# Optimization experiments

Measured on AMD Instinct MI355X. Metric: run time of the kernel, lower is better.

## Reference

```python
import jax, jax.numpy as jnp
import numpy as np

B = 16
PATCH_NUM = 32      # L of inter branch
PATCH_SIZE = 128    # L of intra branch
WIN_SIZE = PATCH_NUM * PATCH_SIZE  # 4096
H = 8
E = 64


def setup_inputs() -> dict:
    key = jax.random.key(0)
    ks = jax.random.split(key, 6)
    return {
        "q_inter": jax.random.normal(ks[0], (B, PATCH_NUM, H, E), jnp.float32),
        "k_inter": jax.random.normal(ks[1], (B, PATCH_NUM, H, E), jnp.float32),
        "v_inter": jax.random.normal(ks[2], (B, PATCH_NUM, H, E), jnp.float32),
        "q_intra": jax.random.normal(ks[3], (B, PATCH_SIZE, H, E), jnp.float32),
        "k_intra": jax.random.normal(ks[4], (B, PATCH_SIZE, H, E), jnp.float32),
        "v_intra": jax.random.normal(ks[5], (B, PATCH_SIZE, H, E), jnp.float32),
    }


def _full_attention(q, k, v):
    # q,k,v: [B, L, H, E]; full softmax attention, scale = 1/sqrt(E)
    scale = 1.0 / jnp.sqrt(jnp.asarray(q.shape[-1], q.dtype))
    score = jnp.einsum('blhe,bshe->bhls', q, k) * scale
    att = jax.nn.softmax(score, axis=-1)  # dropout is identity in eval mode
    return jnp.einsum('bhls,bshd->blhd', att, v)


def reference(q_inter, k_inter, v_inter, q_intra, k_intra, v_intra):
    V_inter = _full_attention(q_inter, k_inter, v_inter)  # [B, patch_num, H, E]
    V_intra = _full_attention(q_intra, k_intra, v_intra)  # [B, patch_size, H, E]
    # einops repeat 'b pn h d -> b (pn ps) h d': each patch repeated ps times
    V_inter_up = jnp.repeat(V_inter, PATCH_SIZE, axis=1)  # [B, win_size, H, E]
    # einops repeat 'b ps h d -> b (ps pn) h d': each position repeated pn times
    V_intra_up = jnp.repeat(V_intra, PATCH_NUM, axis=1)   # [B, win_size, H, E]
    return V_inter_up + V_intra_up
```

## Files before the change

kernel.cpp:

```cpp
#include <hip/hip_runtime.h>


#define NH 8
#define NE 64
#define ROWSTRIDE (NH * NE)

__device__ __forceinline__ float dot4(const float4 a, const float4 b) {
    return a.x * b.x + a.y * b.y + a.z * b.z + a.w * b.w;
}

template <int L, bool FUSED>
__global__ __launch_bounds__(256) void attn_kernel(
    const float* __restrict__ qg_, const float* __restrict__ kg_,
    const float* __restrict__ vg_, float* __restrict__ dst,
    const float* __restrict__ vinter)
{
    constexpr int TILES = L / 32;
    constexpr int CPT   = L / 32;
    constexpr int SST   = L + 1;
    constexpr int KST   = 68;

    __shared__ __align__(16) float Ks[L * KST];
    __shared__ __align__(16) float Vs[L * KST];
    __shared__ __align__(16) float Qs[32 * KST];
    __shared__ float S[32 * SST];

    const int tid  = threadIdx.x;
    const int bid  = blockIdx.x;
    const int tile = bid % TILES;
    const int h    = (bid / TILES) % NH;
    const int b    = bid / (TILES * NH);
    const int r0   = tile * 32;

    const float* kg = kg_ + ((size_t)b * L * NH + h) * NE;
    const float* vg = vg_ + ((size_t)b * L * NH + h) * NE;
    const float* qg = qg_ + ((size_t)(b * L + r0) * NH + h) * NE;

    for (int idx = tid; idx < L * 16; idx += 256) {
        const int row = idx >> 4;
        const int f   = (idx & 15) * 4;
        *(float4*)&Ks[row * KST + f] = *(const float4*)(kg + (size_t)row * ROWSTRIDE + f);
        *(float4*)&Vs[row * KST + f] = *(const float4*)(vg + (size_t)row * ROWSTRIDE + f);
    }
    for (int idx = tid; idx < 32 * 16; idx += 256) {
        const int row = idx >> 4;
        const int f   = (idx & 15) * 4;
        *(float4*)&Qs[row * KST + f] = *(const float4*)(qg + (size_t)row * ROWSTRIDE + f);
    }
    __syncthreads();

    {
        const int rg = tid >> 5;
        const int cg = tid & 31;
        const int rr = rg * 4;
        const int c0 = cg * CPT;
        float acc[4][CPT];
        #pragma unroll
        for (int i = 0; i < 4; i++)
            #pragma unroll
            for (int j = 0; j < CPT; j++) acc[i][j] = 0.f;

        #pragma unroll
        for (int e = 0; e < NE; e += 4) {
            float4 qv[4], kv[CPT];
            #pragma unroll
            for (int i = 0; i < 4; i++) qv[i] = *(const float4*)&Qs[(rr + i) * KST + e];
            #pragma unroll
            for (int j = 0; j < CPT; j++) kv[j] = *(const float4*)&Ks[(c0 + j) * KST + e];
            #pragma unroll
            for (int i = 0; i < 4; i++)
                #pragma unroll
                for (int j = 0; j < CPT; j++)
                    acc[i][j] += dot4(qv[i], kv[j]);
        }
        #pragma unroll
        for (int i = 0; i < 4; i++)
            #pragma unroll
            for (int j = 0; j < CPT; j++)
                S[(rr + i) * SST + c0 + j] = acc[i][j] * 0.125f;
    }
    __syncthreads();

    const int r   = tid >> 3;
    const int sub = tid & 7;
    float m = -1e30f;
    for (int c = 0; c < L; c++) m = fmaxf(m, S[r * SST + c]);
    float sum = 0.f;
    for (int c = 0; c < L; c++) sum += __expf(S[r * SST + c] - m);
    const float inv = 1.f / sum;
    __syncthreads();
    for (int c = sub; c < L; c += 8)
        S[r * SST + c] = __expf(S[r * SST + c] - m);
    __syncthreads();

    const int e0 = sub * 8;
    float a0=0,a1=0,a2=0,a3=0,a4=0,a5=0,a6=0,a7=0;
    for (int c = 0; c < L; c++) {
        const float p  = S[r * SST + c];
        const float4 va = *(const float4*)&Vs[c * KST + e0];
        const float4 vb = *(const float4*)&Vs[c * KST + e0 + 4];
        a0 += p * va.x; a1 += p * va.y; a2 += p * va.z; a3 += p * va.w;
        a4 += p * vb.x; a5 += p * vb.y; a6 += p * vb.z; a7 += p * vb.w;
    }
    float4 oA = make_float4(a0 * inv, a1 * inv, a2 * inv, a3 * inv);
    float4 oB = make_float4(a4 * inv, a5 * inv, a6 * inv, a7 * inv);

    if (!FUSED) {
        float* w = dst + ((size_t)(b * 32 + r0 + r) * NH + h) * NE + e0;
        *(float4*)w       = oA;
        *(float4*)(w + 4) = oB;
    } else {
        const int i = r0 + r;
        const float* wi = vinter + ((size_t)(b * 32 + (i >> 2)) * NH + h) * NE + e0;
        const float4 iA = *(const float4*)wi;
        const float4 iB = *(const float4*)(wi + 4);
        oA.x += iA.x; oA.y += iA.y; oA.z += iA.z; oA.w += iA.w;
        oB.x += iB.x; oB.y += iB.y; oB.z += iB.z; oB.w += iB.w;
        float* ob = dst + ((size_t)(b * 4096 + i * 32) * NH + h) * NE + e0;
        #pragma unroll
        for (int j = 0; j < 32; j++) {
            *(float4*)(ob + (size_t)j * ROWSTRIDE)     = oA;
            *(float4*)(ob + (size_t)j * ROWSTRIDE + 4) = oB;
        }
    }
}

extern "C" void kernel_launch(void* const* d_in, const int* in_sizes, int n_in,
                              void* d_out, int out_size, void* d_ws, size_t ws_size,
                              hipStream_t stream) {
    const float* q_inter = (const float*)d_in[0];
    const float* k_inter = (const float*)d_in[1];
    const float* v_inter = (const float*)d_in[2];
    const float* q_intra = (const float*)d_in[3];
    const float* k_intra = (const float*)d_in[4];
    const float* v_intra = (const float*)d_in[5];
    float* out = (float*)d_out;
    float* ws  = (float*)d_ws;

    attn_kernel<32, false><<<16 * 8, 256, 0, stream>>>(
        q_inter, k_inter, v_inter, ws, nullptr);

    attn_kernel<128, true><<<16 * 8 * 4, 256, 0, stream>>>(
        q_intra, k_intra, v_intra, out, ws);
}
```

Measured before the change: 194.3 us.

## Split fused upsample-add epilogue into separate coalesced broadcast kernel

The intra attention kernel no longer adds the inter result and writes 32 replicated output rows per thread. Both attention kernels now write compact results to workspace. A new grid-stride kernel with many blocks reads them and writes the full upsampled output with contiguous float4 stores. The aim is to turn the large output write, which dominates traffic, from a strided pattern spread over few blocks into a coalesced one across the whole GPU. The cost is an extra kernel launch and an extra small round-trip through workspace.

```diff
diff --git a/kernel.cpp b/kernel.cpp
--- a/kernel.cpp
+++ b/kernel.cpp
@@ -9,11 +9,10 @@
     return a.x * b.x + a.y * b.y + a.z * b.z + a.w * b.w;
 }
 
-template <int L, bool FUSED>
+template <int L>
 __global__ __launch_bounds__(256) void attn_kernel(
     const float* __restrict__ qg_, const float* __restrict__ kg_,
-    const float* __restrict__ vg_, float* __restrict__ dst,
-    const float* __restrict__ vinter)
+    const float* __restrict__ vg_, float* __restrict__ dst)
 {
     constexpr int TILES = L / 32;
     constexpr int CPT   = L / 32;
@@ -102,26 +101,29 @@
         a0 += p * va.x; a1 += p * va.y; a2 += p * va.z; a3 += p * va.w;
         a4 += p * vb.x; a5 += p * vb.y; a6 += p * vb.z; a7 += p * vb.w;
     }
-    float4 oA = make_float4(a0 * inv, a1 * inv, a2 * inv, a3 * inv);
-    float4 oB = make_float4(a4 * inv, a5 * inv, a6 * inv, a7 * inv);
+    const float4 oA = make_float4(a0 * inv, a1 * inv, a2 * inv, a3 * inv);
+    const float4 oB = make_float4(a4 * inv, a5 * inv, a6 * inv, a7 * inv);
 
-    if (!FUSED) {
-        float* w = dst + ((size_t)(b * 32 + r0 + r) * NH + h) * NE + e0;
-        *(float4*)w       = oA;
-        *(float4*)(w + 4) = oB;
-    } else {
-        const int i = r0 + r;
-        const float* wi = vinter + ((size_t)(b * 32 + (i >> 2)) * NH + h) * NE + e0;
-        const float4 iA = *(const float4*)wi;
-        const float4 iB = *(const float4*)(wi + 4);
-        oA.x += iA.x; oA.y += iA.y; oA.z += iA.z; oA.w += iA.w;
-        oB.x += iB.x; oB.y += iB.y; oB.z += iB.z; oB.w += iB.w;
-        float* ob = dst + ((size_t)(b * 4096 + i * 32) * NH + h) * NE + e0;
-        #pragma unroll
-        for (int j = 0; j < 32; j++) {
-            *(float4*)(ob + (size_t)j * ROWSTRIDE)     = oA;
-            *(float4*)(ob + (size_t)j * ROWSTRIDE + 4) = oB;
-        }
+    float* w = dst + ((size_t)(b * L + r0 + r) * NH + h) * NE + e0;
+    *(float4*)w       = oA;
+    *(float4*)(w + 4) = oB;
+}
+
+__global__ __launch_bounds__(256) void upsample_add_kernel(
+    const float4* __restrict__ wsI, const float4* __restrict__ wsT,
+    float4* __restrict__ out)
+{
+    const int total = 16 * 4096 * NH * (NE / 4);
+    int t = blockIdx.x * 256 + threadIdx.x;
+    const int stride = gridDim.x * 256;
+    for (; t < total; t += stride) {
+        const int e4 = t & 15;
+        const int h  = (t >> 4) & 7;
+        const int l  = (t >> 7) & 4095;
+        const int b  = t >> 19;
+        const float4 a = wsI[((b * 32  + (l >> 7)) * NH + h) * 16 + e4];
+        const float4 c = wsT[((b * 128 + (l >> 5)) * NH + h) * 16 + e4];
+        out[t] = make_float4(a.x + c.x, a.y + c.y, a.z + c.z, a.w + c.w);
     }
 }
 
@@ -135,11 +137,13 @@
     const float* k_intra = (const float*)d_in[4];
     const float* v_intra = (const float*)d_in[5];
     float* out = (float*)d_out;
-    float* ws  = (float*)d_ws;
+    float* wsI = (float*)d_ws;
+    float* wsT = wsI + (size_t)16 * 32 * NH * NE;
 
-    attn_kernel<32, false><<<16 * 8, 256, 0, stream>>>(
-        q_inter, k_inter, v_inter, ws, nullptr);
+    attn_kernel<32><<<16 * 8, 256, 0, stream>>>(q_inter, k_inter, v_inter, wsI);
 
-    attn_kernel<128, true><<<16 * 8 * 4, 256, 0, stream>>>(
-        q_intra, k_intra, v_intra, out, ws);
+    attn_kernel<128><<<16 * 8 * 4, 256, 0, stream>>>(q_intra, k_intra, v_intra, wsT);
+
+    upsample_add_kernel<<<8192, 256, 0, stream>>>(
+        (const float4*)wsI, (const float4*)wsT, (float4*)out);
 }
```

New measurement: 194.6 us. About the same (+0.2%).
